# Performance work log

Measured on AMD Instinct MI355X. Metric: run time of the kernel, lower is better.

## Reference

```python
import jax, jax.numpy as jnp
import numpy as np


def setup_inputs() -> dict:
    key = jax.random.key(0)
    B, V, U = 4096, 256, 128
    # x[b, t, j]: weight of matching arriving node t of batch b to fixed node j-1;
    # column 0 is the 'skip' option (weight forced to 0 inside reference).
    x = jax.random.normal(key, (B, V, U + 1), dtype=jnp.float32)
    return {"x": x, "u_size": U, "v_size": V, "skip_steps": 25}


def reference(x, u_size, v_size, skip_steps):
    """Greedy online bipartite matching decode (model 'greedy-m').

    Sequentially processes v_size arriving nodes. For the first `skip_steps`
    steps (threshold phase) it always selects action 0 (skip). Afterwards it
    greedily matches the arriving node to the highest-weight still-available
    u node (action 0 = skip, weight 0, always available). Returns
    (-total_matching_weight, sequence_of_selected_actions) mirroring
    (-state.size, torch.stack(sequences, 1)).
    """
    B = x.shape[0]
    NEG = jnp.asarray(-1e30, dtype=x.dtype)
    w = x.at[:, :, 0].set(0.0)  # skip option has zero weight
    u_ids = jnp.arange(u_size + 1)  # [U+1]

    def step(carry, inp):
        mask, size = carry          # mask: [B, U+1] bool (True = already matched)
        w_t, i = inp                # w_t: [B, U+1]
        avail = jnp.where(mask, NEG, w_t)
        sel = jnp.where(i < skip_steps, 0, jnp.argmax(avail, axis=-1))  # [B]
        chosen = jnp.take_along_axis(w_t, sel[:, None], axis=-1)[:, 0]
        size = size + chosen
        new_mask = mask | (u_ids[None, :] == sel[:, None])
        new_mask = new_mask.at[:, 0].set(False)  # skip never exhausted
        return (new_mask, size), sel

    mask0 = jnp.zeros((B, u_size + 1), dtype=bool)
    size0 = jnp.zeros((B,), dtype=x.dtype)
    (_, size), pi = jax.lax.scan(
        step, (mask0, size0), (jnp.swapaxes(w, 0, 1), jnp.arange(v_size))
    )
    pi = jnp.swapaxes(pi, 0, 1)  # [B, V]
    return (-size, pi)
```

## Files before the change

### kernel.cpp

```cpp
#include <hip/hip_runtime.h>


__device__ __forceinline__ unsigned int fkey(float f) {
    unsigned int u = __float_as_uint(f);
    return u ^ ((unsigned int)((int)u >> 31) | 0x80000000u);
}

__device__ __forceinline__ float fkey_inv(unsigned int k) {
    return __uint_as_float((k & 0x80000000u) ? (k ^ 0x80000000u) : ~k);
}

__global__ __launch_bounds__(256, 4) void greedy_match_kernel(
    const float* __restrict__ x,
    float* __restrict__ out,
    int B)
{
    const int V = 256;
    const int SKIP = 25;
    const int ROWLEN = 129;
    const unsigned int KZERO = 0x80000000u;

    int gtid = blockIdx.x * blockDim.x + threadIdx.x;
    int w = gtid >> 6;
    int lane = gtid & 63;
    if (w >= B) return;

    const float* p = x + (size_t)w * V * ROWLEN + (size_t)SKIP * ROWLEN;
    float* out_pi = out + B + (size_t)w * V;

    float acc = 0.0f;
    float pi_val = 0.0f;
    unsigned int mask = 0;

    float w0 = p[1 + lane];
    float w1 = p[65 + lane];

    for (int t = SKIP; t < V; ++t) {
        const float* pn = p + ((t + 1 < V) ? ROWLEN : 0);
        float nw0 = pn[1 + lane];
        float nw1 = pn[65 + lane];

        unsigned int f0 = (mask & 1u) ? 0u : fkey(w0);
        unsigned int f1 = (mask & 2u) ? 0u : fkey(w1);
        unsigned int k = max(max(f0, f1), KZERO);
        #pragma unroll
        for (int off = 32; off > 0; off >>= 1) {
            unsigned int o = __shfl_xor(k, off, 64);
            k = max(k, o);
        }

        int sel;
        if (k == KZERO) {
            sel = 0;
        } else {
            unsigned long long b0 = __ballot(f0 == k);
            if (b0) {
                sel = __ffsll(b0);
            } else {
                unsigned long long b1 = __ballot(f1 == k);
                sel = __ffsll(b1) + 64;
            }
        }

        acc += fkey_inv(k);

        if (sel == lane + 1)       mask |= 1u;
        else if (sel == lane + 65) mask |= 2u;

        if (lane == (t & 63)) pi_val = (float)sel;
        if ((t & 63) == 63) out_pi[(t & ~63) + lane] = pi_val;

        w0 = nw0; w1 = nw1;
        p += ROWLEN;
    }

    if (lane == 0) out[w] = -acc;
}

extern "C" void kernel_launch(void* const* d_in, const int* in_sizes, int n_in,
                              void* d_out, int out_size, void* d_ws, size_t ws_size,
                              hipStream_t stream) {
    const float* x = (const float*)d_in[0];
    const int V = 256, ROWLEN = 129;
    int B = in_sizes[0] / (V * ROWLEN);
    float* out = (float*)d_out;

    int threads = 256;
    int blocks = (B * 64 + threads - 1) / threads;
    greedy_match_kernel<<<blocks, threads, 0, stream>>>(x, out, B);
}
```

Measured before the change: 734.2 us.

## Use DPP float max reduction and deepen row prefetch to two steps

Replaces the shuffle-based wave max over order-preserving integer keys with a float max built from DPP row and broadcast steps plus a readlane, removing the key encode and decode. Both ballots are now issued unconditionally instead of branching. The weight prefetch is deepened from one row ahead to two, to hide more global load latency in the serial per-step loop. The cost is more live registers, and NaN or ±0 corner cases may differ slightly from the integer-key compare.

```diff
diff --git a/kernel.cpp b/kernel.cpp
--- a/kernel.cpp
+++ b/kernel.cpp
@@ -1,13 +1,21 @@
 #include <hip/hip_runtime.h>
 
 
-__device__ __forceinline__ unsigned int fkey(float f) {
-    unsigned int u = __float_as_uint(f);
-    return u ^ ((unsigned int)((int)u >> 31) | 0x80000000u);
+template <int CTRL>
+__device__ __forceinline__ float maxstep(float v) {
+    float t = __int_as_float(__builtin_amdgcn_update_dpp(
+        __float_as_int(v), __float_as_int(v), CTRL, 0xF, 0xF, false));
+    return fmaxf(v, t);
 }
 
-__device__ __forceinline__ float fkey_inv(unsigned int k) {
-    return __uint_as_float((k & 0x80000000u) ? (k ^ 0x80000000u) : ~k);
+__device__ __forceinline__ float wave_max_bcast(float v) {
+    v = maxstep<0x111>(v);
+    v = maxstep<0x112>(v);
+    v = maxstep<0x114>(v);
+    v = maxstep<0x118>(v);
+    v = maxstep<0x142>(v);
+    v = maxstep<0x143>(v);
+    return __int_as_float(__builtin_amdgcn_readlane(__float_as_int(v), 63));
 }
 
 __global__ __launch_bounds__(256, 4) void greedy_match_kernel(
@@ -18,51 +26,43 @@
     const int V = 256;
     const int SKIP = 25;
     const int ROWLEN = 129;
-    const unsigned int KZERO = 0x80000000u;
+    const float NEG = -1e30f;
 
     int gtid = blockIdx.x * blockDim.x + threadIdx.x;
     int w = gtid >> 6;
     int lane = gtid & 63;
     if (w >= B) return;
 
-    const float* p = x + (size_t)w * V * ROWLEN + (size_t)SKIP * ROWLEN;
+    const float* base = x + (size_t)w * V * ROWLEN;
     float* out_pi = out + B + (size_t)w * V;
 
     float acc = 0.0f;
     float pi_val = 0.0f;
     unsigned int mask = 0;
 
-    float w0 = p[1 + lane];
-    float w1 = p[65 + lane];
+    float w0a = base[(size_t)SKIP * ROWLEN + 1 + lane];
+    float w1a = base[(size_t)SKIP * ROWLEN + 65 + lane];
+    float w0b = base[(size_t)(SKIP + 1) * ROWLEN + 1 + lane];
+    float w1b = base[(size_t)(SKIP + 1) * ROWLEN + 65 + lane];
 
     for (int t = SKIP; t < V; ++t) {
-        const float* pn = p + ((t + 1 < V) ? ROWLEN : 0);
-        float nw0 = pn[1 + lane];
-        float nw1 = pn[65 + lane];
+        int tp = t + 2; if (tp > V - 1) tp = V - 1;
+        const float* pp = base + (size_t)tp * ROWLEN;
+        float nw0 = pp[1 + lane];
+        float nw1 = pp[65 + lane];
 
-        unsigned int f0 = (mask & 1u) ? 0u : fkey(w0);
-        unsigned int f1 = (mask & 2u) ? 0u : fkey(w1);
-        unsigned int k = max(max(f0, f1), KZERO);
-        #pragma unroll
-        for (int off = 32; off > 0; off >>= 1) {
-            unsigned int o = __shfl_xor(k, off, 64);
-            k = max(k, o);
+        float a0 = (mask & 1u) ? NEG : w0a;
+        float a1 = (mask & 2u) ? NEG : w1a;
+        float m = fmaxf(fmaxf(a0, a1), 0.0f);
+        float k = wave_max_bcast(m);
+
+        int sel = 0;
+        if (k > 0.0f) {
+            unsigned long long b0 = __ballot(a0 == k);
+            unsigned long long b1 = __ballot(a1 == k);
+            sel = b0 ? __ffsll(b0) : (__ffsll(b1) + 64);
         }
-
-        int sel;
-        if (k == KZERO) {
-            sel = 0;
-        } else {
-            unsigned long long b0 = __ballot(f0 == k);
-            if (b0) {
-                sel = __ffsll(b0);
-            } else {
-                unsigned long long b1 = __ballot(f1 == k);
-                sel = __ffsll(b1) + 64;
-            }
-        }
-
-        acc += fkey_inv(k);
+        acc += k;
 
         if (sel == lane + 1)       mask |= 1u;
         else if (sel == lane + 65) mask |= 2u;
@@ -70,8 +70,7 @@
         if (lane == (t & 63)) pi_val = (float)sel;
         if ((t & 63) == 63) out_pi[(t & ~63) + lane] = pi_val;
 
-        w0 = nw0; w1 = nw1;
-        p += ROWLEN;
+        w0a = w0b; w1a = w1b; w0b = nw0; w1b = nw1;
     }
 
     if (lane == 0) out[w] = -acc;
```

After: 737.0 us. No clear change (+0.4%).
